# Kernel tuning notes

Hardware: AMD Instinct MI355X
Metric: run time of the kernel (lower is better)

## Reference

```python
import jax, jax.numpy as jnp
import numpy as np
from jax import lax

V, D, H, L = 128, 1024, 1024, 2
B, T = 64, 512


def setup_inputs() -> dict:
    key = jax.random.key(0)
    ks = jax.random.split(key, 8)
    s = 0.05
    return {
        "x": jax.random.randint(ks[0], (B, T), 0, V),
        "embed": jax.random.normal(ks[1], (V, D), jnp.float32) * s,
        "Wx": jax.random.normal(ks[2], (L, 4 * H, D), jnp.float32) * s,
        "Wh": jax.random.normal(ks[3], (L, 4 * H, H), jnp.float32) * s,
        "b": jax.random.normal(ks[4], (L, 4 * H), jnp.float32) * s,
        "Wout": jax.random.normal(ks[5], (V, H), jnp.float32) * s,
        "bout": jax.random.normal(ks[6], (V,), jnp.float32) * s,
    }


def _lstm_step(Wx, Wh, b, carry, x_t):
    # carry: (h[L,B,H], c[L,B,H]); x_t: [B,D]
    h, c = carry
    inp = x_t
    hs, cs = [], []
    for l in range(L):
        gates = inp @ Wx[l].T + h[l] @ Wh[l].T + b[l]  # [B,4H]
        i, f, g, o = jnp.split(gates, 4, axis=-1)
        c_new = jax.nn.sigmoid(f) * c[l] + jax.nn.sigmoid(i) * jnp.tanh(g)
        h_new = jax.nn.sigmoid(o) * jnp.tanh(c_new)
        hs.append(h_new)
        cs.append(c_new)
        inp = h_new
    return (jnp.stack(hs), jnp.stack(cs)), inp


def reference(x, embed, Wx, Wh, b, Wout, bout):
    emb = embed[x]                      # [B,T,D]
    xs = jnp.swapaxes(emb, 0, 1)        # [T,B,D] for scan over time
    h0 = jnp.zeros((L, B, H), emb.dtype)
    c0 = jnp.zeros((L, B, H), emb.dtype)
    step = lambda carry, x_t: _lstm_step(Wx, Wh, b, carry, x_t)
    _, outs = lax.scan(step, (h0, c0), xs)  # outs: [T,B,H] (top-layer h)
    outs = jnp.swapaxes(outs, 0, 1)         # [B,T,H]
    logits = outs @ Wout.T + bout           # [B,T,V]
    return logits
```

## Files before the change

kernel.cpp:

```cpp
#include <hip/hip_runtime.h>
#include <hip/hip_bf16.h>

constexpr int cV = 128, cD = 1024, cH = 1024, cB = 64, cT = 512;
constexpr int c4H = 4096;
constexpr int NBLK = 256;
constexpr int FSTR = 32;

typedef __attribute__((ext_vector_type(8))) short bf16x8;
typedef __attribute__((ext_vector_type(4))) float f32x4;
typedef __attribute__((ext_vector_type(4))) int i32x4;

__device__ __forceinline__ short f2b(float f) {
  __hip_bfloat16 h = __float2bfloat16(f);
  return __builtin_bit_cast(short, h);
}
__device__ __forceinline__ float sigf(float x) { return 1.0f / (1.0f + __expf(-x)); }

__device__ __forceinline__ void gload16(const short* g, short* l) {
  __builtin_amdgcn_global_load_lds(
      (const __attribute__((address_space(1))) void*)g,
      (__attribute__((address_space(3))) void*)l, 16, 0, 0);
}

__global__ void cvt_bf16_kernel(const float* __restrict__ src, short* __restrict__ dst, int n8) {
  int q = blockIdx.x * blockDim.x + threadIdx.x;
  if (q >= n8) return;
  const float4* s = (const float4*)src + (size_t)q * 2;
  float4 a = s[0], b = s[1];
  union { short s8[8]; int4 v; } u;
  u.s8[0] = f2b(a.x); u.s8[1] = f2b(a.y); u.s8[2] = f2b(a.z); u.s8[3] = f2b(a.w);
  u.s8[4] = f2b(b.x); u.s8[5] = f2b(b.y); u.s8[6] = f2b(b.z); u.s8[7] = f2b(b.w);
  *(int4*)(dst + (size_t)q * 8) = u.v;
}

struct RParams {
  const float* Wx;
  const float* Wh;
  const float* bias;
  const int*   x;
  const short* embedb;
  short* h0hist;
  short* outs;
  const short* zpage;
  int* flags;
};

__launch_bounds__(512, 1)
__global__ void lstm_recurrent(RParams P) {
  __shared__ __align__(16) short S0[32768];
  __shared__ __align__(16) short S1[32768];
  __shared__ float pLDS[8][32][17];
  __shared__ float cLDS[512];
  __shared__ float bLDS[2][32];
  __shared__ short hLDS[512];

  const int tid = threadIdx.x;
  const int lane = tid & 63, wv = tid >> 6;
  const int l15 = lane & 15, lhi = lane >> 4;
  const int op = wv & 3;
  const int ns = wv >> 2;
  const int blk = blockIdx.x;
  const int slice = blk & 127;
  const int bh = blk >> 7;
  const int hc0 = slice * 8;
  int* F = P.flags;
  const int fbase = bh * 128;

  bf16x8 w[32];
  {
    const float* Wsrc = ((op & 1) ? P.Wh : P.Wx) + (size_t)(op >> 1) * c4H * cD;
    int r = ns * 16 + l15;
    const float* base = Wsrc + (size_t)((r >> 3) * cH + hc0 + (r & 7)) * cD + lhi * 8;
    #pragma unroll
    for (int kt = 0; kt < 32; ++kt) {
      float4 a = *(const float4*)(base + kt * 32);
      float4 b = *(const float4*)(base + kt * 32 + 4);
      union { short s8[8]; bf16x8 v; } u;
      u.s8[0] = f2b(a.x); u.s8[1] = f2b(a.y); u.s8[2] = f2b(a.z); u.s8[3] = f2b(a.w);
      u.s8[4] = f2b(b.x); u.s8[5] = f2b(b.y); u.s8[6] = f2b(b.z); u.s8[7] = f2b(b.w);
      w[kt] = u.v;
    }
  }
  if (tid < 64) {
    int l = tid >> 5, r = tid & 31;
    bLDS[l][r] = P.bias[l * c4H + (r >> 3) * cH + hc0 + (r & 7)];
  }
  cLDS[tid] = 0.0f;
  __syncthreads();

  f32x4 accx[2] = {};
  if (op == 0) {
    int v0 = P.x[(bh * 32 + l15) * cT + 0];
    int v1 = P.x[(bh * 32 + 16 + l15) * cT + 0];
    const short* e0 = P.embedb + (size_t)v0 * 1024 + lhi * 8;
    const short* e1 = P.embedb + (size_t)v1 * 1024 + lhi * 8;
    #pragma unroll
    for (int kt = 0; kt < 32; ++kt) {
      bf16x8 a0 = *(const bf16x8*)(e0 + kt * 32);
      bf16x8 a1 = *(const bf16x8*)(e1 + kt * 32);
      accx[0] = __builtin_amdgcn_mfma_f32_16x16x32_bf16(a0, w[kt], accx[0], 0, 0, 0);
      accx[1] = __builtin_amdgcn_mfma_f32_16x16x32_bf16(a1, w[kt], accx[1], 0, 0, 0);
    }
  }

  for (int p = 0; p <= cT; ++p) {
    const bool l0act = (p < cT);
    const bool l1act = (p >= 1);
    const short* s0g = P.h0hist + (size_t)p * 65536;
    const short* s1g = (p >= 2) ? (P.outs + (size_t)(p - 2) * 65536) : P.zpage;

    if (wv == 7) {
      bool done = false;
      while (!done) {
        int a0 = __hip_atomic_load(&F[(fbase + lane) * FSTR],
                                   __ATOMIC_RELAXED, __HIP_MEMORY_SCOPE_AGENT);
        int a1 = __hip_atomic_load(&F[(fbase + 64 + lane) * FSTR],
                                   __ATOMIC_RELAXED, __HIP_MEMORY_SCOPE_AGENT);
        done = __all(a0 >= p && a1 >= p);
        if (!done) __builtin_amdgcn_s_sleep(1);
      }
    }
    __syncthreads();

    #pragma unroll
    for (int j = 0; j < 8; ++j) {
      int s = tid + j * 512;
      int oct = s >> 5, row = s & 31;
      const short* gsrc = s0g + oct * 512 + bh * 256 + row * 8;
      gload16(gsrc, S0 + s * 8);
      const short* gsrc1 = s1g + oct * 512 + bh * 256 + row * 8;
      gload16(gsrc1, S1 + s * 8);
    }
    __syncthreads();

    f32x4 acc[2];
    if (op == 0) {
      acc[0] = accx[0]; acc[1] = accx[1];
    } else {
      acc[0] = (f32x4){0.f, 0.f, 0.f, 0.f};
      acc[1] = (f32x4){0.f, 0.f, 0.f, 0.f};
      const short* S = (op == 3) ? S1 : S0;
      const short* lb = S + lhi * 256 + l15 * 8;
      #pragma unroll
      for (int kt = 0; kt < 32; ++kt) {
        bf16x8 a0 = *(const bf16x8*)(lb + kt * 1024);
        bf16x8 a1 = *(const bf16x8*)(lb + kt * 1024 + 128);
        acc[0] = __builtin_amdgcn_mfma_f32_16x16x32_bf16(a0, w[kt], acc[0], 0, 0, 0);
        acc[1] = __builtin_amdgcn_mfma_f32_16x16x32_bf16(a1, w[kt], acc[1], 0, 0, 0);
      }
    }
    #pragma unroll
    for (int mi = 0; mi < 2; ++mi)
      #pragma unroll
      for (int v = 0; v < 4; ++v)
        pLDS[wv][mi * 16 + lhi * 4 + v][l15] = acc[mi][v];
    __syncthreads();

    {
      int l = tid >> 8, b = (tid >> 3) & 31, hc = tid & 7;
      bool act = l ? l1act : l0act;
      if (act) {
        float gt[4];
        #pragma unroll
        for (int g = 0; g < 4; ++g) {
          int r = g * 8 + hc;
          int wB = (r >> 4) * 4 + 2 * l;
          gt[g] = pLDS[wB][b][r & 15] + pLDS[wB + 1][b][r & 15] + bLDS[l][r];
        }
        float cold = cLDS[tid];
        float cn = sigf(gt[1]) * cold + sigf(gt[0]) * tanhf(gt[2]);
        float hn = sigf(gt[3]) * tanhf(cn);
        cLDS[tid] = cn;
        hLDS[tid] = f2b(hn);
      }
    }
    __syncthreads();

    if (wv == 0) {
      bool doStore = (lane < 32) ? l0act : l1act;
      if (doStore) {
        short* d = (lane < 32)
            ? (P.h0hist + (size_t)(p + 1) * 65536 + slice * 512 + bh * 256 + (lane & 31) * 8)
            : (P.outs   + (size_t)(p - 1) * 65536 + slice * 512 + bh * 256 + (lane & 31) * 8);
        i32x4 hv = *(const i32x4*)&hLDS[lane * 8];
        asm volatile("global_store_dwordx4 %0, %1, off sc0 sc1" :: "v"(d), "v"(hv) : "memory");
      }
      asm volatile("s_waitcnt vmcnt(0)" ::: "memory");
      if (lane == 0)
        __hip_atomic_store(&F[blk * FSTR], p + 1, __ATOMIC_RELAXED, __HIP_MEMORY_SCOPE_AGENT);
    }

    if (op == 0) {
      accx[0] = (f32x4){0.f, 0.f, 0.f, 0.f};
      accx[1] = (f32x4){0.f, 0.f, 0.f, 0.f};
      if (p + 1 < cT) {
        int t = p + 1;
        int v0 = P.x[(bh * 32 + l15) * cT + t];
        int v1 = P.x[(bh * 32 + 16 + l15) * cT + t];
        const short* e0 = P.embedb + (size_t)v0 * 1024 + lhi * 8;
        const short* e1 = P.embedb + (size_t)v1 * 1024 + lhi * 8;
        #pragma unroll
        for (int kt = 0; kt < 32; ++kt) {
          bf16x8 a0 = *(const bf16x8*)(e0 + kt * 32);
          bf16x8 a1 = *(const bf16x8*)(e1 + kt * 32);
          accx[0] = __builtin_amdgcn_mfma_f32_16x16x32_bf16(a0, w[kt], accx[0], 0, 0, 0);
          accx[1] = __builtin_amdgcn_mfma_f32_16x16x32_bf16(a1, w[kt], accx[1], 0, 0, 0);
        }
      }
    }
  }
}

__launch_bounds__(256, 1)
__global__ void proj_kernel(const short* __restrict__ outs, const short* __restrict__ Woutb,
                            const float* __restrict__ bout, float* __restrict__ logits) {
  const int tid = threadIdx.x, lane = tid & 63, wv = tid >> 6;
  const int l15 = lane & 15, lhi = lane >> 4;
  const int t = blockIdx.x;
  const int row = wv * 16 + l15;
  const short* Abase = outs + (size_t)t * 65536;
  f32x4 acc[8] = {};
  for (int k = 0; k < 1024; k += 32) {
    bf16x8 af = *(const bf16x8*)(Abase + ((k >> 3) + lhi) * 512 + row * 8);
    #pragma unroll
    for (int nn = 0; nn < 8; ++nn) {
      bf16x8 bf = *(const bf16x8*)(Woutb + (size_t)(nn * 16 + l15) * 1024 + k + lhi * 8);
      acc[nn] = __builtin_amdgcn_mfma_f32_16x16x32_bf16(af, bf, acc[nn], 0, 0, 0);
    }
  }
  #pragma unroll
  for (int nn = 0; nn < 8; ++nn) {
    #pragma unroll
    for (int v = 0; v < 4; ++v) {
      int b = wv * 16 + lhi * 4 + v;
      int col = nn * 16 + l15;
      logits[(size_t)b * (cT * cV) + (size_t)t * cV + col] = acc[nn][v] + bout[col];
    }
  }
}

extern "C" void kernel_launch(void* const* d_in, const int* in_sizes, int n_in,
                              void* d_out, int out_size, void* d_ws, size_t ws_size,
                              hipStream_t stream) {
  const int* x = (const int*)d_in[0];
  const float* embed = (const float*)d_in[1];
  const float* Wx = (const float*)d_in[2];
  const float* Wh = (const float*)d_in[3];
  const float* bias = (const float*)d_in[4];
  const float* Wout = (const float*)d_in[5];
  const float* bout = (const float*)d_in[6];
  float* logits = (float*)d_out;

  char* ws = (char*)d_ws;
  size_t off = 0;
  auto alloc = [&](size_t bytes) {
    char* p = ws + off;
    off += (bytes + 255) & ~(size_t)255;
    return p;
  };
  short* Woutb  = (short*)alloc((size_t)cV * cH * 2);
  short* embedb = (short*)alloc((size_t)cV * cD * 2);
  short* outs   = (short*)alloc((size_t)cT * 65536 * 2);
  short* h0hist = (short*)alloc((size_t)(cT + 1) * 65536 * 2);
  char* state0 = ws + off;
  short* zpage  = (short*)alloc((size_t)65536 * 2);
  int* flags    = (int*)alloc((size_t)NBLK * FSTR * sizeof(int));
  size_t state_bytes = (size_t)((ws + off) - state0);

  hipMemsetAsync(state0, 0, state_bytes, stream);
  hipMemsetAsync(h0hist, 0, (size_t)65536 * 2, stream);

  int n8 = cV * cH / 8;
  cvt_bf16_kernel<<<(n8 + 255) / 256, 256, 0, stream>>>(Wout, Woutb, n8);
  cvt_bf16_kernel<<<(n8 + 255) / 256, 256, 0, stream>>>(embed, embedb, n8);

  RParams P{Wx, Wh, bias, x, embedb, h0hist, outs, zpage, flags};
  lstm_recurrent<<<dim3(NBLK), dim3(512), 0, stream>>>(P);

  proj_kernel<<<cT, 256, 0, stream>>>(outs, Woutb, bout, logits);
}
```

Baseline: 4.226 ms.

## Stage hidden-state chunks into LDS as soon as each producer flag is ready

Replaces the wait-for-all-flags barrier followed by a bulk global-to-LDS copy with per-chunk staging. Two waves poll the producer flags, and each issues its LDS loads for a chunk pair once that pair's flags are set. This overlaps the copy with waiting on slower producers and removes one block barrier per step. In exchange, the copy work that was spread over all 512 threads now runs on two waves, and the loop issues more small, serialized load batches.

Measured after the change: 4.220 ms. About the same (-0.1%).

```diff
diff --git a/kernel.cpp b/kernel.cpp
--- a/kernel.cpp
+++ b/kernel.cpp
@@ -109,27 +109,27 @@
     const short* s0g = P.h0hist + (size_t)p * 65536;
     const short* s1g = (p >= 2) ? (P.outs + (size_t)(p - 2) * 65536) : P.zpage;
 
-    if (wv == 7) {
-      bool done = false;
-      while (!done) {
-        int a0 = __hip_atomic_load(&F[(fbase + lane) * FSTR],
-                                   __ATOMIC_RELAXED, __HIP_MEMORY_SCOPE_AGENT);
-        int a1 = __hip_atomic_load(&F[(fbase + 64 + lane) * FSTR],
-                                   __ATOMIC_RELAXED, __HIP_MEMORY_SCOPE_AGENT);
-        done = __all(a0 >= p && a1 >= p);
-        if (!done) __builtin_amdgcn_s_sleep(1);
-      }
-    }
-    __syncthreads();
-
-    #pragma unroll
-    for (int j = 0; j < 8; ++j) {
-      int s = tid + j * 512;
-      int oct = s >> 5, row = s & 31;
-      const short* gsrc = s0g + oct * 512 + bh * 256 + row * 8;
-      gload16(gsrc, S0 + s * 8);
-      const short* gsrc1 = s1g + oct * 512 + bh * 256 + row * 8;
-      gload16(gsrc1, S1 + s * 8);
+    if (wv >= 6) {
+      const int* fa = &F[(fbase + 2 * lane) * FSTR];
+      const int* fb = &F[(fbase + 2 * lane + 1) * FSTR];
+      const short* gsrc = (wv == 7) ? s0g : s1g;
+      short* ldst = (wv == 7) ? S0 : S1;
+      unsigned long long staged = 0ull;
+      while (staged != ~0ull) {
+        int va = __hip_atomic_load(fa, __ATOMIC_RELAXED, __HIP_MEMORY_SCOPE_AGENT);
+        int vb = __hip_atomic_load(fb, __ATOMIC_RELAXED, __HIP_MEMORY_SCOPE_AGENT);
+        unsigned long long m = __ballot(va >= p && vb >= p) & ~staged;
+        if (!m) { __builtin_amdgcn_s_sleep(1); continue; }
+        staged |= m;
+        while (m) {
+          int c = __builtin_ctzll(m);
+          m &= m - 1;
+          int oct = 2 * c + (lane >> 5);
+          int row = lane & 31;
+          gload16(gsrc + oct * 512 + bh * 256 + row * 8, ldst + (c * 64 + lane) * 8);
+        }
+      }
+      asm volatile("s_waitcnt vmcnt(0)" ::: "memory");
     }
     __syncthreads();
 
```
